# Optimization experiments

Hardware: AMD Instinct MI355X
Metric: run time of the kernel (lower is better)

## Reference

```python
import jax, jax.numpy as jnp
import numpy as np

DT = 1e-3
TAU_MEM_INV = 100.0
TAU_SYN_INV = 200.0
TAU_PRE_INV = 20.0
TAU_POST_INV = 20.0
ETA_PLUS, ETA_MINUS = 0.004, 0.003
W_MIN, W_MAX = 0.0, 1.0


def _dog_kernels():
    # DoGFilter.DoG_kernel(sigma1=1, sigma2=2, size=5): ax = arange(-2, 3)
    ax = jnp.arange(-2.0, 3.0)
    xx, yy = jnp.meshgrid(ax, ax, indexing='ij')
    r2 = xx * xx + yy * yy
    g1 = jnp.exp(-r2 / 2.0)
    g1 = g1 / g1.sum()
    g2 = jnp.exp(-r2 / 8.0)
    g2 = g2 / g2.sum()
    return g1[None, None], g2[None, None]


def _conv(x, w):
    # torch Conv2d (cross-correlation), stride 1, no padding
    return jax.lax.conv_general_dilated(x, w, (1, 1), 'VALID', dimension_numbers=('NCHW', 'OIHW', 'NCHW'))


def _maxpool2(x):
    return jax.lax.reduce_window(x, -jnp.inf, jax.lax.max, (1, 1, 2, 2), (1, 1, 2, 2), 'VALID')


def _unfold(x, k):
    # torch.nn.functional.unfold: [B,C,H,W] -> [B, C*k*k, L], channel-major (c, kh, kw)
    B, C, H, W = x.shape
    Ho, Wo = H - k + 1, W - k + 1
    cols = jnp.stack([x[:, :, i:i + Ho, j:j + Wo] for i in range(k) for j in range(k)], axis=2)
    return cols.reshape(B, C * k * k, Ho * Wo)


def _lif_step(inp, v, i, v_th):
    # norse lif_feed_forward_step (v_leak = v_reset = 0); forward spike = heaviside
    v_dec = v + DT * TAU_MEM_INV * (-v + i)
    i_dec = i - DT * TAU_SYN_INV * i
    z = (v_dec - v_th > 0).astype(inp.dtype)
    return z, (1.0 - z) * v_dec, i_dec + inp


def _stdp_step(z_pre, z_post, w, t_pre, t_post):
    # norse stdp_step_conv2d with stdp_algorithm='multiplicative_relu', mu=0, hard bounds [0,1]
    t_pre = t_pre + DT * TAU_PRE_INV * (-t_pre + z_pre)
    t_post = t_post + DT * TAU_POST_INV * (-t_post + z_post)
    k = w.shape[2]
    B, Co = z_post.shape[0], z_post.shape[1]
    zp = z_post.reshape(B, Co, -1)
    tp = t_post.reshape(B, Co, -1)
    dw_plus = ETA_PLUS * jax.nn.relu(W_MAX - w) * jnp.einsum('bil,bjl->ji', _unfold(t_pre, k), zp).reshape(w.shape)
    dw_minus = ETA_MINUS * jax.nn.relu(w - W_MIN) * jnp.einsum('bil,bjl->ji', _unfold(z_pre, k), tp).reshape(w.shape)
    w = jnp.clip(w + dw_plus - dw_minus, W_MIN, W_MAX)
    return w, t_pre, t_post


def _forward(x, dog_b1, dog_b2, w1, w2, fc1_w, fc1_b, out_w):
    T, B, _, H, _ = x.shape
    g1, g2 = _dog_kernels()
    Hd = H - 4          # DoG output (60)
    H1 = Hd - 4         # conv1 output (56)
    Hp = H1 // 2        # pooled (28)
    H2 = Hp - 4         # conv2 output (24)
    Bf = (B * 100) // 3200  # rows after z4.view(-1, 3200)
    f32 = x.dtype
    z0 = lambda *s: jnp.zeros(s, f32)
    carry = (w1, w2,
             z0(B, 30, H1, H1), z0(B, 30, H1, H1),     # lif0 v, i
             z0(B, 100, H2, H2), z0(B, 100, H2, H2),   # lif1 v, i
             z0(Bf, 500), z0(Bf, 500),                 # lif2 v, i
             z0(Bf, 10), z0(Bf, 10),                   # LI output cell v, i
             z0(B, 2, Hd, Hd), z0(B, 30, H1, H1),      # stdp1 t_pre, t_post
             z0(B, 30, Hp, Hp), z0(B, 100, H2, H2))    # stdp2 t_pre, t_post

    def step(c, xt):
        (w1, w2, v0, i0, v1, i1, v2, i2, vo, io, tp1, tq1, tp2, tq2) = c
        # DoG filter: the two Conv2d biases survive the weight overwrite
        x1 = _conv(xt, g1) + dog_b1
        x2 = _conv(xt, g2) + dog_b2
        z = jnp.concatenate([x1 - x2, x2 - x1], axis=1)   # on/off channels [B,2,Hd,Hd]
        z2 = _conv(z, w1)
        z2, v0, i0 = _lif_step(z2, v0, i0, 15.0)
        w1, tp1, tq1 = _stdp_step(z, z2, w1, tp1, tq1)
        z3 = _maxpool2(z2)
        z4 = 10.0 * _conv(z3, w2)
        z4, v1, i1 = _lif_step(z4, v1, i1, 10.0)
        w2, tp2, tq2 = _stdp_step(z3, z4, w2, tp2, tq2)
        g = jnp.max(z4, axis=(2, 3)).reshape(-1, 3200)    # AdaptiveMaxPool2d(1) + view(-1, 3200)
        h = g @ fc1_w.T + fc1_b
        h, v2, i2 = _lif_step(h, v2, i2, 1.0)
        # LILinearCell (norse li_step), no bias
        i_jump = io + jax.nn.relu(h) @ out_w.T
        vo = vo + DT * TAU_MEM_INV * (-vo + i_jump)
        io = i_jump - DT * TAU_SYN_INV * i_jump
        volt = jnp.broadcast_to(vo, (B, 10))              # voltages[ts] = v (broadcast [1,10] -> [B,10])
        return (w1, w2, v0, i0, v1, i1, v2, i2, vo, io, tp1, tq1, tp2, tq2), volt

    _, voltages = jax.lax.scan(jax.checkpoint(step), carry, x)
    return voltages  # [T, B, 10]


def setup_inputs() -> dict:
    key = jax.random.key(0)
    ks = jax.random.split(key, 7)
    T, B, H = 32, 32, 64
    return {
        'x': jax.random.uniform(ks[0], (T, B, 1, H, H), jnp.float32),
        'dog_b1': jax.random.uniform(ks[1], (1,), jnp.float32, -0.2, 0.2),
        'dog_b2': jax.random.uniform(ks[2], (1,), jnp.float32, -0.2, 0.2),
        'w1': jax.random.normal(ks[3], (30, 2, 5, 5), jnp.float32),
        'w2': jax.random.normal(ks[4], (100, 30, 5, 5), jnp.float32),
        'fc1_w': jax.random.normal(ks[5], (500, 3200), jnp.float32) * 0.02,
        'fc1_b': jnp.zeros((500,), jnp.float32),
        'out_w': jax.random.normal(ks[6], (10, 500), jnp.float32) * float(np.sqrt(2.0 / 500.0)),
    }


def reference(x, dog_b1, dog_b2, w1, w2, fc1_w, fc1_b, out_w):
    return _forward(x, dog_b1, dog_b2, w1, w2, fc1_w, fc1_b, out_w)
```

## Files before the change

### kernel.cpp

```cpp
#include <hip/hip_runtime.h>
#include <math.h>

#define DTMEM 0.1f
#define DTSYN 0.2f
#define DTTR  0.02f

static constexpr int B = 32, T = 32;
static constexpr int HD = 60, HP = 28;
static constexpr int LD = HD*HD, LP = HP*HP;

static constexpr size_t SVI = (size_t)B*8*2*7*448*4;
static constexpr size_t SST = (size_t)B*8*2*7*448*2;
static constexpr size_t S2  = (size_t)B*7*6*384*4;

static constexpr size_t OW1A  = 0;
static constexpr size_t OW1B  = OW1A + 1500;
static constexpr size_t OVI0  = OW1B + 1500;
static constexpr size_t OTQ1  = OVI0 + SVI;
static constexpr size_t OTP2  = OTQ1 + SST;
static constexpr size_t OZ3A  = OTP2 + (size_t)B*30*LP;
static constexpr size_t OZ3B  = OZ3A + (size_t)B*30*LP;
static constexpr size_t OV1S  = OZ3B + (size_t)B*30*LP;
static constexpr size_t OI1S  = OV1S + S2;
static constexpr size_t OTQ2S = OI1S + S2;
static constexpr size_t OPHIA = OTQ2S + S2;
static constexpr size_t OPLOA = OPHIA + 376320;
static constexpr size_t OPZ3A = OPLOA + 376320;
static constexpr size_t OPHIB = OPZ3A + 376320;
static constexpr size_t OPLOB = OPHIB + 376320;
static constexpr size_t OPZ3B = OPLOB + 376320;
static constexpr size_t OZEROEND = OPZ3B + 376320;
static constexpr size_t OZALL  = OZEROEND;
static constexpr size_t OTPALL = OZALL + (size_t)T*B*3600;
static constexpr size_t OEPA  = OTPALL + (size_t)T*B*3600;
static constexpr size_t OEMA  = OEPA + (size_t)B*75000;
static constexpr size_t OEPB  = OEMA + (size_t)B*75000;
static constexpr size_t OEMB  = OEPB + (size_t)B*75000;
static constexpr size_t OPARTA = OEMB + (size_t)B*75000;
static constexpr size_t OPARTB = OPARTA + 96000;
static constexpr size_t OG    = OPARTB + 96000;
static constexpr size_t OHH   = OG + (size_t)T*3200;
static constexpr size_t OW2A  = OHH + (size_t)T*500;
static constexpr size_t OW2B  = OW2A + 84000;
static constexpr size_t OCNZA = OW2B + 84000;
static constexpr size_t OCNZB = OCNZA + 3840;
static constexpr size_t OQZF  = OCNZB + 3840;
static constexpr size_t OPZF  = OQZF + 512;
static constexpr size_t OSZF  = OPZF + 960;
static constexpr size_t OEAA  = OSZF + 224;
static constexpr size_t OEAB  = OEAA + 224;
static constexpr size_t OATH  = OEAB + 224;
static constexpr size_t OATL  = OATH + 516096;
static constexpr size_t OSPK  = OATL + 516096;
static constexpr size_t OEND  = OSPK + 16;

struct DK { float v[25]; };

typedef __attribute__((ext_vector_type(8))) short bfx8;
typedef __attribute__((ext_vector_type(4))) float f32x4;

static __device__ __forceinline__ unsigned short f2bf(float f) {
    unsigned u = __float_as_uint(f);
    return (unsigned short)((u + 0x7FFFu + ((u >> 16) & 1u)) >> 16);
}
static __device__ __forceinline__ float bf2f(unsigned short h) {
    return __uint_as_float(((unsigned)h) << 16);
}

static __device__ __forceinline__ float2 w1pair(const float* w1cur, const float* pprev,
                                                int o, int pp, int t) {
    float wa = w1cur[o*50 + pp], wb = w1cur[o*50 + 25 + pp];
    if (t > 0) {
        float EpS = 0.f, EmS = 0.f;
        for (int s = 0; s < 64; ++s) {
            EpS += pprev[s*1500 + o*50 + pp];
            EmS += pprev[s*1500 + o*50 + 25 + pp];
        }
        wa = fminf(fmaxf(wa + 0.004f*fmaxf(1.f-wa,0.f)*EpS - 0.003f*fmaxf(wa,0.f)*EmS, 0.f), 1.f);
        wb = fminf(fmaxf(wb + 0.004f*fmaxf(1.f-wb,0.f)*(-EpS) - 0.003f*fmaxf(wb,0.f)*(-EmS), 0.f), 1.f);
    }
    return make_float2(wa, wb);
}

static __device__ __forceinline__ float w2eff(float w, int e, int jgg,
        const int* eaR, const float* EPr, const float* EMr) {
    float ep = 0.f, em = 0.f; int any = 0;
    for (int bb = 0; bb < 32; ++bb) {
        if (eaR[bb*7 + jgg]) {
            any = 1;
            ep += EPr[(size_t)bb*75000 + e];
            em += EMr[(size_t)bb*75000 + e];
        }
    }
    if (!any) return w;
    float dwp = 0.004f * fmaxf(1.0f - w, 0.0f) * ep;
    float dwm = 0.003f * fmaxf(w, 0.0f) * em;
    return fminf(fmaxf(w + dwp - dwm, 0.0f), 1.0f);
}

union SMEM {
    struct {
        float zsh[32*60];
        float tsh[32*60];
        float red[700];
        float wd[100];
        float vish[448*4];
        float tqsh[448*2];
        int   sflags[8];
    } f;
    struct {
        union { float spre[LP]; unsigned short sB[10656]; } u;
        unsigned short aTH[8*576], aTL[8*576];
        unsigned int aZ4b[16*18];
        int sjany[16];
        int sany, sAnyTq, ganyJ;
        int sCA[30];
    } v;
};

__global__ __launch_bounds__(384) void k_pre(
        const float* __restrict__ x, const float* __restrict__ b1,
        const float* __restrict__ b2, float* __restrict__ zall,
        float* __restrict__ tpall, DK dk) {
    __shared__ __attribute__((aligned(16))) float xsh[10*64];
    int g = blockIdx.x, b = blockIdx.y, tid = threadIdx.x;
    int r0 = g*6;
    bool valid = tid < 360;
    int lr = tid / 60, col = tid - lr*60;
    float tp = 0.f;
    float bias = b1[0] - b2[0];
    #pragma unroll 1
    for (int t = 0; t < T; ++t) {
        __syncthreads();
        const float4* xs = (const float4*)(x + ((size_t)t*B + b)*4096 + (size_t)r0*64);
        for (int i = tid; i < 160; i += 384) ((float4*)xsh)[i] = xs[i];
        __syncthreads();
        if (valid) {
            float a = 0.f;
            #pragma unroll
            for (int kh = 0; kh < 5; kh++)
                #pragma unroll
                for (int kw = 0; kw < 5; kw++)
                    a = fmaf(dk.v[kh*5+kw], xsh[(lr+kh)*64 + col + kw], a);
            float zv = a + bias;
            tp = tp + DTTR*(zv - tp);
            size_t o = ((size_t)t*B + b)*3600 + (size_t)g*360 + tid;
            zall[o] = zv;
            tpall[o] = tp;
        }
    }
}

__global__ __launch_bounds__(448) void k_sim(
        const float* __restrict__ zall, const float* __restrict__ w1,
        int* __restrict__ spk) {
    __shared__ __attribute__((aligned(16))) float zsh[32*60];
    __shared__ float wd0[100], wdC[100];
    const int og = blockIdx.x & 7, by = blockIdx.x >> 3;
    const int b = by >> 1, yh = by & 1, y0 = yh*28;
    const int tid = threadIdx.x;
    if (tid < 100) {
        int oo2 = tid / 25, pp = tid % 25;
        int o2 = og*4 + oo2; if (o2 > 29) o2 = 29;
        float wa = w1[o2*50 + pp], wb = w1[o2*50 + 25 + pp];
        wd0[tid] = wa - wb;
        wa = fminf(fmaxf(wa, 0.f), 1.f);
        wb = fminf(fmaxf(wb, 0.f), 1.f);
        wdC[tid] = wa - wb;
    }
    int oo = tid & 3, xq = (tid >> 2) & 3, yv = tid >> 4;
    int o = og*4 + oo, xx0 = xq*14;
    bool valid = (o < 30);
    float v[14], ci[14];
    #pragma unroll
    for (int k = 0; k < 14; ++k) { v[k] = 0.f; ci[k] = 0.f; }
    bool any = false;
    #pragma unroll 1
    for (int t = 0; t < T; ++t) {
        __syncthreads();
        const float4* zs = (const float4*)(zall + ((size_t)t*B + b)*3600 + (size_t)y0*60);
        for (int i2 = tid; i2 < 480; i2 += 448) ((float4*)zsh)[i2] = zs[i2];
        __syncthreads();
        if (valid) {
            float acc[14];
            #pragma unroll
            for (int k = 0; k < 14; k++) acc[k] = 0.f;
            const float* wdp = (t == 0) ? wd0 : wdC;
            #pragma unroll
            for (int kh = 0; kh < 5; kh++) {
                float rr[18];
                const float2* r2 = (const float2*)&zsh[(yv+kh)*HD + xx0];
                #pragma unroll
                for (int i = 0; i < 9; i++) ((float2*)rr)[i] = r2[i];
                #pragma unroll
                for (int kw = 0; kw < 5; kw++) {
                    float w = wdp[oo*25 + kh*5 + kw];
                    #pragma unroll
                    for (int k = 0; k < 14; k++) acc[k] = fmaf(w, rr[k+kw], acc[k]);
                }
            }
            #pragma unroll
            for (int e = 0; e < 14; ++e) {
                float vd = v[e] + DTMEM*(ci[e] - v[e]);
                float z = (vd > 15.0f) ? 1.0f : 0.0f;
                any = any || (z != 0.f);
                v[e] = (1.0f - z)*vd;
                ci[e] = (ci[e] - DTSYN*ci[e]) + acc[e];
            }
        }
    }
    if (any) atomicOr(spk, 1);
}

__global__ __launch_bounds__(448) void k_step(float* __restrict__ ws, int t) {
    __shared__ __attribute__((aligned(16))) SMEM sm;
    const int blk = blockIdx.x, tid = threadIdx.x;
    if (((const int*)(ws + OSPK))[0] == 0) return;

    if (blk < 224) {
        const int u = t - 1;
        if (u < 0) return;
        const int cb = blk;
        const int jgg = cb % 7, b = cb / 7, jb0 = jgg*16;
        const float* w2cur = ws + ((u&1) ? OW2B : OW2A);
        float*       w2nxt = ws + ((u&1) ? OW2A : OW2B);
        const float* EPr = ws + ((u&1) ? OEPA : OEPB);
        const float* EMr = ws + ((u&1) ? OEMA : OEMB);
        float*       EPw = ws + ((u&1) ? OEPB : OEPA);
        float*       EMw = ws + ((u&1) ? OEMB : OEMA);
        const int*   eaR = (const int*)(ws + ((u&1) ? OEAA : OEAB));
        int*         eaW = (int*)(ws + ((u&1) ? OEAB : OEAA));
        const int*   cnzP = (const int*)(ws + ((u&1) ? OCNZB : OCNZA));
        const float* z3r = ws + ((u&1) ? OZ3B : OZ3A);
        const unsigned short* uhiR = (const unsigned short*)(ws + ((u&1) ? OPHIB : OPHIA));
        const unsigned short* uloR = (const unsigned short*)(ws + ((u&1) ? OPLOB : OPLOA));
        const unsigned short* uz3R = (const unsigned short*)(ws + ((u&1) ? OPZ3B : OPZ3A));
        unsigned short* gTH = (unsigned short*)(ws + OATH) + (size_t)cb*8*576;
        unsigned short* gTL = (unsigned short*)(ws + OATL) + (size_t)cb*8*576;
        int* szf = (int*)(ws + OSZF);
        float* g_t = ws + OG + (size_t)u*3200;

        if (u < 31) {
            int e = cb*448 + tid;
            if (e < 75000) {
                int j = e/750, r = e - j*750, c = r/25, p25 = r - c*25;
                size_t f = ((size_t)j*30 + c)*28 + p25;
                float w = w2cur[f];
                if (u >= 1) w = w2eff(w, e, j>>4, eaR, EPr, EMr);
                w2nxt[f] = w;
            }
        }

        if (tid == 0) { sm.v.sany = 0; sm.v.sAnyTq = 0; sm.v.ganyJ = 0; }
        if (tid < 16) sm.v.sjany[tid] = 0;
        for (int i2 = tid; i2 < 288; i2 += 448) sm.v.aZ4b[i2] = 0u;
        __syncthreads();
        if (tid < 120 && cnzP[b*120 + tid]) atomicOr(&sm.v.sany, 1);
        if (tid < 30) {
            const int* cz = cnzP + (b*30 + tid)*4;
            sm.v.sCA[tid] = (cz[0] | cz[1] | cz[2] | cz[3]);
        }
        if (u >= 1 && tid < 32 && eaR[tid*7 + jgg]) atomicOr(&sm.v.ganyJ, 1);
        __syncthreads();
        const int szv = szf[b*7 + jgg];
        if (szv && !sm.v.sany) {
            if (tid < 16 && jb0 + tid < 100) g_t[b*100 + jb0 + tid] = 0.f;
            if (u < 31 && tid == 0) eaW[b*7 + jgg] = 0;
            return;
        }
        const bool run = tid < 384;
        int jp = tid & 7, xh = (tid >> 3) & 1, yv = tid >> 4;
        int j0 = jb0 + jp*2;
        int ja = (j0 < 100) ? j0 : 99, jbb = (j0+1 < 100) ? j0+1 : 99;
        int xx0 = xh*12;
        float acc0[12], acc1[12];
        #pragma unroll
        for (int xq = 0; xq < 12; xq++) { acc0[xq] = 0.f; acc1[xq] = 0.f; }
        const int gJ = sm.v.ganyJ;
        #pragma unroll 1
        for (int c = 0; c < 30; ++c) {
            bool act = sm.v.sCA[c] != 0;
            __syncthreads();
            if (act) {
                const float4* src = (const float4*)(z3r + (size_t)(b*30 + c)*LP);
                for (int i2 = tid; i2 < 196; i2 += 448) ((float4*)sm.v.u.spre)[i2] = src[i2];
            }
            __syncthreads();
            if (!act) continue;
            if (run) {
                #pragma unroll 1
                for (int jj = 0; jj < 2; ++jj) {
                    int jc = jj ? jbb : ja;
                    float wa[28];
                    #pragma unroll
                    for (int i = 0; i < 7; i++)
                        ((float4*)wa)[i] = ((const float4*)(w2cur + ((size_t)jc*30 + c)*28))[i];
                    if (u >= 1 && gJ) {
                        #pragma unroll
                        for (int p25 = 0; p25 < 25; p25++)
                            wa[p25] = w2eff(wa[p25], (jc*30 + c)*25 + p25, jc>>4, eaR, EPr, EMr);
                    }
                    float* accp = jj ? acc1 : acc0;
                    #pragma unroll
                    for (int kh = 0; kh < 5; kh++) {
                        float rr[16];
                        const float4* r4 = (const float4*)&sm.v.u.spre[(yv+kh)*HP + xx0];
                        #pragma unroll
                        for (int i = 0; i < 4; i++) ((float4*)rr)[i] = r4[i];
                        #pragma unroll
                        for (int kw = 0; kw < 5; kw++) {
                            float w0 = wa[kh*5+kw];
                            #pragma unroll
                            for (int xq = 0; xq < 12; xq++)
                                accp[xq] = fmaf(w0, rr[xq+kw], accp[xq]);
                        }
                    }
                }
            }
        }
        bool spk0 = false, spk1 = false, anyTq = false;
        if (run) {
            float4* v1p = (float4*)(ws + OV1S);
            float4* i1p = (float4*)(ws + OI1S);
            float4* t2p = (float4*)(ws + OTQ2S);
            size_t sb2 = ((size_t)(b*7 + jgg)*6)*384 + tid;
            #pragma unroll
            for (int jj = 0; jj < 2; jj++) {
                bool anyspk = false;
                int rj = jp*2 + jj;
                #pragma unroll
                for (int i = 0; i < 3; i++) {
                    size_t si = sb2 + (size_t)(jj*3 + i)*384;
                    float4 v4 = v1p[si];
                    float4 c4 = i1p[si];
                    float4 t4 = t2p[si];
                    float4 vn, in, tn4;
                    float* vp=(float*)&v4; float* cp=(float*)&c4; float* tp=(float*)&t4;
                    float* vnp=(float*)&vn; float* inp=(float*)&in; float* tnp=(float*)&tn4;
                    unsigned zb4 = 0;
                    #pragma unroll
                    for (int k = 0; k < 4; k++) {
                        float a = jj ? acc1[i*4+k] : acc0[i*4+k];
                        float vd = vp[k] + DTMEM*(cp[k] - vp[k]);
                        float z = (vd > 10.0f) ? 1.0f : 0.0f;
                        vnp[k] = (1.0f - z)*vd;
                        inp[k] = (cp[k] - DTSYN*cp[k]) + 10.0f*a;
                        tnp[k] = tp[k] + DTTR*(z - tp[k]);
                        if (z != 0.f) { zb4 |= 1u << k; anyspk = true; }
                        anyTq = anyTq || (tnp[k] != 0.f);
                    }
                    v1p[si] = vn;
                    i1p[si] = in;
                    t2p[si] = tn4;
                    int col = yv*24 + xx0 + i*4;
                    if (zb4) atomicOr(&sm.v.aZ4b[rj*18 + (col >> 5)], zb4 << (col & 31));
                    ushort4 hb, lb4;
                    unsigned short h;
                    h = f2bf(tnp[0]); hb.x = h; lb4.x = f2bf(tnp[0] - bf2f(h));
                    h = f2bf(tnp[1]); hb.y = h; lb4.y = f2bf(tnp[1] - bf2f(h));
                    h = f2bf(tnp[2]); hb.z = h; lb4.z = f2bf(tnp[2] - bf2f(h));
                    h = f2bf(tnp[3]); hb.w = h; lb4.w = f2bf(tnp[3] - bf2f(h));
                    if (rj < 8) {
                        *(ushort4*)&sm.v.aTH[rj*576 + col] = hb;
                        *(ushort4*)&sm.v.aTL[rj*576 + col] = lb4;
                    } else {
                        size_t gb = (size_t)(rj - 8)*576 + col;
                        *(ushort4*)(gTH + gb) = hb;
                        *(ushort4*)(gTL + gb) = lb4;
                    }
                }
                if (jj == 0) spk0 = anyspk; else spk1 = anyspk;
            }
            if (spk0 && j0 < 100) atomicOr(&sm.v.sjany[jp*2], 1);
            if (spk1 && j0+1 < 100) atomicOr(&sm.v.sjany[jp*2+1], 1);
            if (anyTq) atomicOr(&sm.v.sAnyTq, 1);
        }
        __syncthreads();
        if (tid < 16 && jb0 + tid < 100) g_t[b*100 + jb0 + tid] = sm.v.sjany[tid] ? 1.f : 0.f;
        if (tid == 0 && szv) szf[b*7 + jgg] = 0;
        if (u < 31) {
            int m0i = 0;
            #pragma unroll
            for (int k = 0; k < 16; k++) m0i |= sm.v.sjany[k];
            bool m0 = (m0i != 0);
            bool mq = (sm.v.sAnyTq != 0);
            bool ea = m0 || mq;
            if (tid == 0) eaW[b*7 + jgg] = ea ? 1 : 0;
            if (!ea) return;
            for (int i2 = tid; i2 < 576; i2 += 448) sm.v.u.sB[10080 + i2] = 0;
            int lane = tid & 63, wv = tid >> 6;
            int mode = wv >> 1, n = wv & 1;
            bool wact = (wv < 4);
            int r = lane & 15;
            bool r8 = (r < 8);
            int g8 = (lane >> 4) * 8;
            int p25 = n*16 + r;
            int offB1, offB2;
            {
                int offH, offL, offZ;
                if (p25 < 25) {
                    int dy = p25/5, dx = p25 - dy*5;
                    offH = ((0*5 + dx)*672 + dy*24)*2;
                    offL = ((1*5 + dx)*672 + dy*24)*2;
                    offZ = ((2*5 + dx)*672 + dy*24)*2;
                } else { offH = offL = offZ = 10080*2; }
                offB1 = (mode == 0) ? offH : offZ;
                offB2 = (mode == 0) ? offL : offZ;
            }
            float* Ew = (mode == 0) ? EPw : EMw;
            const char* sBb = (const char*)sm.v.u.sB;
            #pragma unroll 1
            for (int h = 0; h < 2; ++h) {
                if (h == 1) {
                    __syncthreads();
                    for (int i2 = tid; i2 < 1152; i2 += 448) {
                        if (i2 < 576) ((uint4*)sm.v.aTH)[i2] = ((const uint4*)gTH)[i2];
                        else ((uint4*)sm.v.aTL)[i2-576] = ((const uint4*)gTL)[i2-576];
                    }
                }
                int m0h = sm.v.sjany[h*8+0] | sm.v.sjany[h*8+1] | sm.v.sjany[h*8+2] |
                          sm.v.sjany[h*8+3] | sm.v.sjany[h*8+4] | sm.v.sjany[h*8+5] |
                          sm.v.sjany[h*8+6] | sm.v.sjany[h*8+7];
                #pragma unroll 1
                for (int c = 0; c < 30; ++c) {
                    bool cAc = sm.v.sCA[c] != 0;
                    __syncthreads();
                    {
                        const size_t pbase = (size_t)(b*30 + c)*784;
                        for (int idx = tid; idx < 784; idx += 448) {
                            int rw = idx/28, col = idx - rw*28;
                            #pragma unroll
                            for (int pl = 0; pl < 3; ++pl) {
                                bool need = (pl < 2) ? m0 : (cAc && mq);
                                if (!need) continue;
                                unsigned short vvv =
                                    ((pl == 0) ? uhiR : (pl == 1) ? uloR : uz3R)[pbase + idx];
                                int base = pl*5*672 + rw*24;
                                #pragma unroll
                                for (int dx = 0; dx < 5; ++dx) {
                                    int xx = col - dx;
                                    if (xx >= 0 && xx < 24) sm.v.u.sB[base + dx*672 + xx] = vvv;
                                }
                            }
                        }
                    }
                    __syncthreads();
                    if (!wact) continue;
                    f32x4 C = (f32x4){0.f, 0.f, 0.f, 0.f};
                    bool go = (mode == 0) ? (m0h != 0) : (mq && cAc);
                    if (go) {
                        for (int ks = 0; ks < 18; ++ks) {
                            int kk = ks*32 + g8;
                            bfx8 a1 = {}, a2 = {};
                            if (mode == 0) {
                                unsigned wbits = 0;
                                if (r8) wbits = sm.v.aZ4b[(h*8 + r)*18 + ks] >> g8;
                                #pragma unroll
                                for (int k = 0; k < 8; ++k)
                                    ((short*)&a1)[k] = ((wbits >> k) & 1u) ? (short)0x3F80 : (short)0;
                                a2 = a1;
                            } else if (r8) {
                                a1 = *(const bfx8*)(sm.v.aTH + r*576 + ks*32);
                                a2 = *(const bfx8*)(sm.v.aTL + r*576 + ks*32);
                            }
                            bfx8 b1v = *(const bfx8*)(sBb + offB1 + kk*2);
                            bfx8 b2v = *(const bfx8*)(sBb + offB2 + kk*2);
                            C = __builtin_amdgcn_mfma_f32_16x16x32_bf16(a1, b1v, C, 0, 0, 0);
                            C = __builtin_amdgcn_mfma_f32_16x16x32_bf16(a2, b2v, C, 0, 0, 0);
                        }
                    }
                    if (p25 < 25 && (lane >> 4) < 2) {
                        #pragma unroll
                        for (int q = 0; q < 4; ++q) {
                            int j = jb0 + h*8 + (lane >> 4)*4 + q;
                            if (j < 100)
                                Ew[(size_t)b*75000 + ((size_t)j*30 + c)*25 + p25] = C[q];
                        }
                    }
                }
            }
        }
        return;
    }

    if (t >= T) return;
    const int fb = blk - 224;
    const int og = fb & 7, by = fb >> 3;
    const int b = by >> 1, yh = by & 1, y0 = yh*28;

    const float* w1cur = ws + ((t&1) ? OW1B : OW1A);
    float*       w1nxt = ws + ((t&1) ? OW1A : OW1B);
    float*       partW = ws + ((t&1) ? OPARTB : OPARTA);
    const float* pprev = ws + ((t&1) ? OPARTA : OPARTB);
    int*         cnzW  = (int*)(ws + ((t&1) ? OCNZB : OCNZA));
    float*       z3W   = ws + ((t&1) ? OZ3B : OZ3A);
    unsigned short* uhiW = (unsigned short*)(ws + ((t&1) ? OPHIB : OPHIA));
    unsigned short* uloW = (unsigned short*)(ws + ((t&1) ? OPLOB : OPLOA));
    unsigned short* uz3W = (unsigned short*)(ws + ((t&1) ? OPZ3B : OPZ3A));
    float* vi0g = ws + OVI0; float* tq1g = ws + OTQ1;
    float* tp2g = ws + OTP2;
    int* qzf = (int*)(ws + OQZF);
    int* pzf = (int*)(ws + OPZF);

    const int prow = (b*2 + yh)*1500;
    int qzOld = qzf[(b*8 + og)*2 + yh];
    size_t sb = ((size_t)((b*8 + og)*2 + yh)*7)*448 + tid;
    float4* vi0p = (float4*)vi0g;
    float2* tq1p = (float2*)tq1g;
    {
        const float4* zs = (const float4*)(ws + OZALL + ((size_t)t*B + b)*3600 + (size_t)y0*60);
        const float4* ts = (const float4*)(ws + OTPALL + ((size_t)t*B + b)*3600 + (size_t)y0*60);
        for (int i2 = tid; i2 < 480; i2 += 448) {
            ((float4*)sm.f.zsh)[i2] = zs[i2];
            ((float4*)sm.f.tsh)[i2] = ts[i2];
        }
        #pragma unroll
        for (int i = 0; i < 7; i++)
            ((float4*)sm.f.vish)[i*448 + tid] = vi0p[sb + (size_t)i*448];
        if (!qzOld) {
            #pragma unroll
            for (int i = 0; i < 7; i++)
                ((float2*)sm.f.tqsh)[i*448 + tid] = tq1p[sb + (size_t)i*448];
        }
    }
    if (tid < 100) {
        int oo2 = tid / 25, pp = tid % 25;
        int o2 = og*4 + oo2; if (o2 > 29) o2 = 29;
        float2 wp = w1pair(w1cur, pprev, o2, pp, t);
        sm.f.wd[tid] = wp.x - wp.y;
    }
    if (fb < 4) {
        int e = fb*448 + tid;
        if (e < 1500) {
            int o = e/50, r = e%50, ch = r/25, pp = r%25;
            float2 wp = w1pair(w1cur, pprev, o, pp, t);
            w1nxt[e] = ch ? wp.y : wp.x;
        }
    }
    if (tid < 8) sm.f.sflags[tid] = 0;
    __syncthreads();
    int oo = tid & 3, xq = (tid >> 2) & 3, yv = tid >> 4;
    int o = og*4 + oo, xx0 = xq*14;
    bool valid = (o < 30);
    unsigned zmask = 0;
    float qs = 0.f;
    bool anym = false;
    if (valid) {
        float acc[14];
        #pragma unroll
        for (int k = 0; k < 14; k++) acc[k] = 0.f;
        #pragma unroll
        for (int kh = 0; kh < 5; kh++) {
            float rr[18];
            const float2* r2 = (const float2*)&sm.f.zsh[(yv+kh)*HD + xx0];
            #pragma unroll
            for (int i = 0; i < 9; i++) ((float2*)rr)[i] = r2[i];
            #pragma unroll
            for (int kw = 0; kw < 5; kw++) {
                float w = sm.f.wd[oo*25 + kh*5 + kw];
                #pragma unroll
                for (int k = 0; k < 14; k++) acc[k] = fmaf(w, rr[k+kw], acc[k]);
            }
        }
        #pragma unroll
        for (int i = 0; i < 7; i++) {
            float4 vi = ((float4*)sm.f.vish)[i*448 + tid];
            float2 t2;
            if (qzOld) { t2.x = 0.f; t2.y = 0.f; }
            else t2 = ((float2*)sm.f.tqsh)[i*448 + tid];
            float4 vin;
            float2 tn2;
            bool sp = false;
            #pragma unroll
            for (int k = 0; k < 2; k++) {
                int e = i*2 + k;
                float vv = k ? vi.y : vi.x, cc = k ? vi.w : vi.z, tt = k ? t2.y : t2.x;
                float vd = vv + DTMEM*(cc - vv);
                float z = (vd > 15.0f) ? 1.0f : 0.0f;
                float vo = (1.0f - z)*vd;
                float io_ = (cc - DTSYN*cc) + acc[e];
                float tq = tt + DTTR*(z - tt);
                if (k) { vin.y = vo; vin.w = io_; tn2.y = tq; }
                else   { vin.x = vo; vin.z = io_; tn2.x = tq; }
                if (z != 0.f) { zmask |= 1u << e; sp = true; }
                qs += tq;
            }
            vi0p[sb + (size_t)i*448] = vin;
            ((float2*)sm.f.tqsh)[i*448 + tid] = tn2;
            if (!qzOld || sp) tq1p[sb + (size_t)i*448] = tn2;
        }
        float mx[7];
        #pragma unroll
        for (int k = 0; k < 7; k++) mx[k] = ((zmask >> (2*k)) & 3u) ? 1.0f : 0.0f;
        #pragma unroll
        for (int k = 0; k < 7; k++) {
            float pm = __shfl_xor(mx[k], 16, 64);
            mx[k] = fmaxf(mx[k], pm);
        }
        if ((yv & 1) == 0) {
            int pzOld = pzf[b*30 + o];
            int py = yh*14 + (yv >> 1);
            size_t pb = ((size_t)(b*30 + o)*HP + py)*HP + xq*7;
            #pragma unroll
            for (int k = 0; k < 7; k++) {
                float m = mx[k];
                anym = anym || (m != 0.f);
                if (!pzOld || m != 0.f) {
                    z3W[pb + k] = m;
                    float tpv = pzOld ? 0.f : tp2g[pb + k];
                    float tnew = tpv + DTTR*(m - tpv);
                    tp2g[pb + k] = tnew;
                    unsigned short h = f2bf(tnew);
                    uhiW[pb + k] = h;
                    uloW[pb + k] = f2bf(tnew - bf2f(h));
                    uz3W[pb + k] = (m != 0.f) ? (unsigned short)0x3F80 : (unsigned short)0;
                }
            }
        }
    }
    if (anym) atomicOr(&sm.f.sflags[oo*2 + (xq >> 1)], 1);
    __syncthreads();
    int anyblk = sm.f.sflags[0]|sm.f.sflags[1]|sm.f.sflags[2]|sm.f.sflags[3]|
                 sm.f.sflags[4]|sm.f.sflags[5]|sm.f.sflags[6]|sm.f.sflags[7];
    if (tid < 8) {
        int o2 = og*4 + (tid >> 1);
        if (o2 < 30) cnzW[(b*30 + o2)*4 + yh*2 + (tid & 1)] = sm.f.sflags[tid];
    }
    if (tid < 4) {
        int o2 = og*4 + tid;
        if (o2 < 30 && (sm.f.sflags[tid*2] | sm.f.sflags[tid*2+1])) pzf[b*30 + o2] = 0;
    }
    if (tid == 0 && qzOld && anyblk) qzf[(b*8 + og)*2 + yh] = 0;

    if (qzOld && !anyblk) {
        if (tid < 100) {
            int oo2 = tid / 25, q = tid % 25;
            int o2 = og*4 + oo2;
            if (o2 < 30) {
                partW[prow + o2*50 + q] = 0.f;
                partW[prow + o2*50 + 25 + q] = 0.f;
            }
        }
        return;
    }
    int lane = tid & 63, wave = tid >> 6;
    {
        float a[25];
        #pragma unroll
        for (int pq = 0; pq < 25; pq++) a[pq] = 0.f;
        if (valid && qs != 0.f) {
            float tn[14];
            #pragma unroll
            for (int i = 0; i < 7; i++) {
                float2 t2 = ((float2*)sm.f.tqsh)[i*448 + tid];
                tn[2*i] = t2.x; tn[2*i+1] = t2.y;
            }
            #pragma unroll
            for (int kh = 0; kh < 5; kh++) {
                float rr[18];
                const float2* r2 = (const float2*)&sm.f.zsh[(yv+kh)*HD + xx0];
                #pragma unroll
                for (int i = 0; i < 9; i++) ((float2*)rr)[i] = r2[i];
                #pragma unroll
                for (int kw = 0; kw < 5; kw++)
                    #pragma unroll
                    for (int k = 0; k < 14; k++)
                        a[kh*5+kw] = fmaf(rr[k+kw], tn[k], a[kh*5+kw]);
            }
        }
        #pragma unroll
        for (int q = 0; q < 25; q++) {
            float v = a[q];
            v += __shfl_xor(v, 4, 64);
            v += __shfl_xor(v, 8, 64);
            v += __shfl_xor(v, 16, 64);
            v += __shfl_xor(v, 32, 64);
            if (lane < 4) sm.f.red[wave*100 + lane*25 + q] = v;
        }
    }
    __syncthreads();
    if (tid < 100) {
        int oo2 = tid / 25, q = tid % 25;
        float s = 0.f;
        #pragma unroll
        for (int w = 0; w < 7; w++) s += sm.f.red[w*100 + oo2*25 + q];
        int o2 = og*4 + oo2;
        if (o2 < 30) partW[prow + o2*50 + 25 + q] = s;
    }
    __syncthreads();
    {
        float a[25];
        #pragma unroll
        for (int pq = 0; pq < 25; pq++) a[pq] = 0.f;
        if (valid && zmask != 0u) {
            float zf[14];
            #pragma unroll
            for (int k = 0; k < 14; k++) zf[k] = ((zmask >> k) & 1u) ? 1.0f : 0.0f;
            #pragma unroll
            for (int kh = 0; kh < 5; kh++) {
                float rr[18];
                const float2* r2 = (const float2*)&sm.f.tsh[(yv+kh)*HD + xx0];
                #pragma unroll
                for (int i = 0; i < 9; i++) ((float2*)rr)[i] = r2[i];
                #pragma unroll
                for (int kw = 0; kw < 5; kw++)
                    #pragma unroll
                    for (int k = 0; k < 14; k++)
                        a[kh*5+kw] = fmaf(rr[k+kw], zf[k], a[kh*5+kw]);
            }
        }
        #pragma unroll
        for (int q = 0; q < 25; q++) {
            float v = a[q];
            v += __shfl_xor(v, 4, 64);
            v += __shfl_xor(v, 8, 64);
            v += __shfl_xor(v, 16, 64);
            v += __shfl_xor(v, 32, 64);
            if (lane < 4) sm.f.red[wave*100 + lane*25 + q] = v;
        }
    }
    __syncthreads();
    if (tid < 100) {
        int oo2 = tid / 25, q = tid % 25;
        float s = 0.f;
        #pragma unroll
        for (int w = 0; w < 7; w++) s += sm.f.red[w*100 + oo2*25 + q];
        int o2 = og*4 + oo2;
        if (o2 < 30) partW[prow + o2*50 + q] = s;
    }
}

__global__ void k_prep(const float* __restrict__ w2, float* __restrict__ w2p,
                       int* __restrict__ qzf, int* __restrict__ pzf,
                       int* __restrict__ szf, int* __restrict__ spk) {
    int e = blockIdx.x*blockDim.x + threadIdx.x;
    if (e < 75000) {
        int j = e / 750, r = e % 750, c = r / 25, p = r % 25;
        w2p[((size_t)j*30 + c)*28 + p] = w2[e];
    }
    if (e < 512) qzf[e] = 1;
    if (e < 960) pzf[e] = 1;
    if (e < 224) szf[e] = 1;
    if (e < 4) spk[e] = 0;
}

__global__ __launch_bounds__(256) void k_fc1b(
        const float* __restrict__ g_all, const float* __restrict__ fcw,
        const float* __restrict__ fcb, float* __restrict__ h_all) {
    __shared__ float red[8][4];
    int n = blockIdx.x, by = blockIdx.y, tid = threadIdx.x;
    const float4* w4 = (const float4*)(fcw + (size_t)n*3200);
    float4 wreg[4];
    #pragma unroll
    for (int i = 0; i < 4; i++) {
        int k = tid + 256*i;
        if (k < 800) wreg[i] = w4[k];
    }
    float accs[8];
    #pragma unroll
    for (int tt = 0; tt < 8; tt++) accs[tt] = 0.f;
    #pragma unroll 1
    for (int tt = 0; tt < 8; tt++) {
        int t = by*8 + tt;
        const float4* g4 = (const float4*)(g_all + (size_t)t*3200);
        float a = 0.f;
        #pragma unroll
        for (int i = 0; i < 4; i++) {
            int k = tid + 256*i;
            if (k < 800) {
                float4 gv = g4[k];
                a = fmaf(gv.x, wreg[i].x, a);
                a = fmaf(gv.y, wreg[i].y, a);
                a = fmaf(gv.z, wreg[i].z, a);
                a = fmaf(gv.w, wreg[i].w, a);
            }
        }
        accs[tt] = a;
    }
    int lane = tid & 63, wid = tid >> 6;
    #pragma unroll
    for (int tt = 0; tt < 8; tt++) {
        float v = accs[tt];
        #pragma unroll
        for (int s = 32; s >= 1; s >>= 1) v += __shfl_down(v, s, 64);
        if (lane == 0) red[tt][wid] = v;
    }
    __syncthreads();
    if (tid < 8)
        h_all[(size_t)(by*8 + tid)*500 + n] =
            red[tid][0] + red[tid][1] + red[tid][2] + red[tid][3] + fcb[n];
}

__global__ __launch_bounds__(640) void k_head_all(
        const float* __restrict__ h_all, const float* __restrict__ outw,
        float* __restrict__ out) {
    __shared__ float spk[500];
    __shared__ float vout[10];
    int tid = threadIdx.x;
    int wid = tid >> 6, lane = tid & 63;
    float v2r = 0.f, i2r = 0.f;
    float vor = 0.f, ior = 0.f;
    #pragma unroll 1
    for (int t = 0; t < 32; t++) {
        if (tid < 500) {
            float cur = i2r;
            float vd = v2r + DTMEM*(cur - v2r);
            float z = (vd > 1.0f) ? 1.0f : 0.0f;
            v2r = (1.0f - z)*vd;
            i2r = (cur - DTSYN*cur) + h_all[t*500 + tid];
            spk[tid] = z;
        }
        __syncthreads();
        float acc = 0.f;
        for (int n = lane; n < 500; n += 64)
            acc = fmaf(spk[n], outw[wid*500 + n], acc);
        #pragma unroll
        for (int s = 32; s >= 1; s >>= 1) acc += __shfl_down(acc, s, 64);
        if (lane == 0) {
            float ij = ior + acc;
            float vn = vor + DTMEM*(ij - vor);
            ior = ij - DTSYN*ij;
            vor = vn;
            vout[wid] = vn;
        }
        __syncthreads();
        if (tid < 320) out[(size_t)t*320 + tid] = vout[tid % 10];
        __syncthreads();
    }
}

extern "C" void kernel_launch(void* const* d_in, const int* in_sizes, int n_in,
                              void* d_out, int out_size, void* d_ws, size_t ws_size,
                              hipStream_t stream) {
    const float* x    = (const float*)d_in[0];
    const float* b1   = (const float*)d_in[1];
    const float* b2   = (const float*)d_in[2];
    const float* w1   = (const float*)d_in[3];
    const float* w2   = (const float*)d_in[4];
    const float* fcw  = (const float*)d_in[5];
    const float* fcb  = (const float*)d_in[6];
    const float* outw = (const float*)d_in[7];
    float* ws  = (float*)d_ws;
    float* out = (float*)d_out;

    DK dk;
    {
        float g1[25], g2[25], s1 = 0.f, s2 = 0.f;
        for (int i = 0; i < 5; i++)
            for (int j = 0; j < 5; j++) {
                float ai = (float)(i - 2), aj = (float)(j - 2);
                float r2 = ai*ai + aj*aj;
                g1[i*5+j] = expf(-r2/2.0f);
                g2[i*5+j] = expf(-r2/8.0f);
                s1 += g1[i*5+j]; s2 += g2[i*5+j];
            }
        for (int k = 0; k < 25; k++) dk.v[k] = g1[k]/s1 - g2[k]/s2;
    }

    hipMemcpyAsync(ws + OW1A, w1, 1500*sizeof(float), hipMemcpyDeviceToDevice, stream);
    hipMemsetAsync(ws + OVI0, 0, (OZEROEND - OVI0)*sizeof(float), stream);
    hipMemsetAsync(ws + OG, 0, (size_t)T*3200*sizeof(float), stream);
    k_prep<<<294, 256, 0, stream>>>(w2, ws + OW2A, (int*)(ws + OQZF),
                                    (int*)(ws + OPZF), (int*)(ws + OSZF),
                                    (int*)(ws + OSPK));
    k_pre<<<dim3(10, 32), 384, 0, stream>>>(x, b1, b2, ws + OZALL, ws + OTPALL, dk);
    k_sim<<<512, 448, 0, stream>>>(ws + OZALL, ws + OW1A, (int*)(ws + OSPK));

    for (int t = 0; t <= T; ++t)
        k_step<<<736, 448, 0, stream>>>(ws, t);

    k_fc1b<<<dim3(500, 4), 256, 0, stream>>>(ws + OG, fcw, fcb, ws + OHH);
    k_head_all<<<1, 640, 0, stream>>>(ws + OHH, outw, out);
}
```

Before: 338.9 us.

## Gate state zeroing, prep and fc1 on spike flag; double-buffer pre/sim kernels

The spike simulation now runs before state initialisation. The large workspace memset becomes a k_zero kernel that exits when layer 1 produced no spikes. k_prep and k_fc1b also exit early in that case, and k_fc1b then writes just the bias, which matches the result when there is no downstream activity. k_pre and k_sim double-buffer their per-timestep shared-memory tiles, which removes one barrier per step, and k_sim uses 896 threads with 7 outputs each instead of 14. The skip relies on a device-side flag, so the work saved depends on the input, and the reordering adds one extra kernel launch.

```diff
diff --git a/kernel.cpp b/kernel.cpp
--- a/kernel.cpp
+++ b/kernel.cpp
@@ -122,39 +122,46 @@
         const float* __restrict__ x, const float* __restrict__ b1,
         const float* __restrict__ b2, float* __restrict__ zall,
         float* __restrict__ tpall, DK dk) {
-    __shared__ __attribute__((aligned(16))) float xsh[10*64];
+    __shared__ __attribute__((aligned(16))) float xsh[2][10*64];
     int g = blockIdx.x, b = blockIdx.y, tid = threadIdx.x;
     int r0 = g*6;
     bool valid = tid < 360;
     int lr = tid / 60, col = tid - lr*60;
     float tp = 0.f;
     float bias = b1[0] - b2[0];
+    if (tid < 160) {
+        const float4* xs = (const float4*)(x + ((size_t)b)*4096 + (size_t)r0*64);
+        ((float4*)xsh[0])[tid] = xs[tid];
+    }
+    __syncthreads();
     #pragma unroll 1
     for (int t = 0; t < T; ++t) {
-        __syncthreads();
-        const float4* xs = (const float4*)(x + ((size_t)t*B + b)*4096 + (size_t)r0*64);
-        for (int i = tid; i < 160; i += 384) ((float4*)xsh)[i] = xs[i];
-        __syncthreads();
+        const float* xc = xsh[t & 1];
+        if (t + 1 < T && tid < 160) {
+            const float4* xs = (const float4*)(x + ((size_t)(t+1)*B + b)*4096 + (size_t)r0*64);
+            ((float4*)xsh[(t+1) & 1])[tid] = xs[tid];
+        }
         if (valid) {
             float a = 0.f;
             #pragma unroll
             for (int kh = 0; kh < 5; kh++)
                 #pragma unroll
                 for (int kw = 0; kw < 5; kw++)
-                    a = fmaf(dk.v[kh*5+kw], xsh[(lr+kh)*64 + col + kw], a);
+                    a = fmaf(dk.v[kh*5+kw], xc[(lr+kh)*64 + col + kw], a);
             float zv = a + bias;
             tp = tp + DTTR*(zv - tp);
             size_t o = ((size_t)t*B + b)*3600 + (size_t)g*360 + tid;
             zall[o] = zv;
             tpall[o] = tp;
         }
-    }
-}
-
-__global__ __launch_bounds__(448) void k_sim(
+        __syncthreads();
+    }
+}
+
+__global__ __launch_bounds__(896) void k_sim(
         const float* __restrict__ zall, const float* __restrict__ w1,
         int* __restrict__ spk) {
-    __shared__ __attribute__((aligned(16))) float zsh[32*60];
+    __shared__ __attribute__((aligned(16))) float zsh[2][1920];
     __shared__ float wd0[100], wdC[100];
     const int og = blockIdx.x & 7, by = blockIdx.x >> 3;
     const int b = by >> 1, yh = by & 1, y0 = yh*28;
@@ -164,43 +171,50 @@
         int o2 = og*4 + oo2; if (o2 > 29) o2 = 29;
         float wa = w1[o2*50 + pp], wb = w1[o2*50 + 25 + pp];
         wd0[tid] = wa - wb;
-        wa = fminf(fmaxf(wa, 0.f), 1.f);
-        wb = fminf(fmaxf(wb, 0.f), 1.f);
-        wdC[tid] = wa - wb;
-    }
-    int oo = tid & 3, xq = (tid >> 2) & 3, yv = tid >> 4;
-    int o = og*4 + oo, xx0 = xq*14;
+        wdC[tid] = fminf(fmaxf(wa, 0.f), 1.f) - fminf(fmaxf(wb, 0.f), 1.f);
+    }
+    int oo = tid & 3, xq = (tid >> 2) & 7, yv = tid >> 5;
+    int o = og*4 + oo;
     bool valid = (o < 30);
-    float v[14], ci[14];
+    int c0 = xq*7;
+    int cb2 = c0 & ~1;
+    int off = c0 & 1;
+    float v[7], ci[7];
     #pragma unroll
-    for (int k = 0; k < 14; ++k) { v[k] = 0.f; ci[k] = 0.f; }
+    for (int k = 0; k < 7; ++k) { v[k] = 0.f; ci[k] = 0.f; }
     bool any = false;
+    if (tid < 480) {
+        const float4* zs = (const float4*)(zall + ((size_t)b)*3600 + (size_t)y0*60);
+        ((float4*)zsh[0])[tid] = zs[tid];
+    }
+    __syncthreads();
     #pragma unroll 1
     for (int t = 0; t < T; ++t) {
-        __syncthreads();
-        const float4* zs = (const float4*)(zall + ((size_t)t*B + b)*3600 + (size_t)y0*60);
-        for (int i2 = tid; i2 < 480; i2 += 448) ((float4*)zsh)[i2] = zs[i2];
-        __syncthreads();
+        const float* zc = zsh[t & 1];
+        if (t + 1 < T && tid < 480) {
+            const float4* zs = (const float4*)(zall + ((size_t)(t+1)*B + b)*3600 + (size_t)y0*60);
+            ((float4*)zsh[(t+1) & 1])[tid] = zs[tid];
+        }
         if (valid) {
-            float acc[14];
-            #pragma unroll
-            for (int k = 0; k < 14; k++) acc[k] = 0.f;
+            float acc[7];
+            #pragma unroll
+            for (int k = 0; k < 7; k++) acc[k] = 0.f;
             const float* wdp = (t == 0) ? wd0 : wdC;
             #pragma unroll
             for (int kh = 0; kh < 5; kh++) {
-                float rr[18];
-                const float2* r2 = (const float2*)&zsh[(yv+kh)*HD + xx0];
+                float rr[12];
+                const float2* r2 = (const float2*)&zc[(yv+kh)*HD + cb2];
                 #pragma unroll
-                for (int i = 0; i < 9; i++) ((float2*)rr)[i] = r2[i];
+                for (int i = 0; i < 6; i++) ((float2*)rr)[i] = r2[i];
                 #pragma unroll
                 for (int kw = 0; kw < 5; kw++) {
                     float w = wdp[oo*25 + kh*5 + kw];
                     #pragma unroll
-                    for (int k = 0; k < 14; k++) acc[k] = fmaf(w, rr[k+kw], acc[k]);
+                    for (int k = 0; k < 7; k++) acc[k] = fmaf(w, rr[off + k + kw], acc[k]);
                 }
             }
             #pragma unroll
-            for (int e = 0; e < 14; ++e) {
+            for (int e = 0; e < 7; ++e) {
                 float vd = v[e] + DTMEM*(ci[e] - v[e]);
                 float z = (vd > 15.0f) ? 1.0f : 0.0f;
                 any = any || (z != 0.f);
@@ -208,8 +222,19 @@
                 ci[e] = (ci[e] - DTSYN*ci[e]) + acc[e];
             }
         }
+        __syncthreads();
     }
     if (any) atomicOr(spk, 1);
+}
+
+__global__ __launch_bounds__(256) void k_zero(float* __restrict__ ws) {
+    if (((const int*)(ws + OSPK))[0] == 0) return;
+    const size_t n = (OZEROEND - OVI0) / 4;
+    float4* p = (float4*)(ws + OVI0);
+    float4 z; z.x = 0.f; z.y = 0.f; z.z = 0.f; z.w = 0.f;
+    for (size_t i = (size_t)blockIdx.x*blockDim.x + threadIdx.x; i < n;
+         i += (size_t)gridDim.x*blockDim.x)
+        p[i] = z;
 }
 
 __global__ __launch_bounds__(448) void k_step(float* __restrict__ ws, int t) {
@@ -732,7 +757,8 @@
 
 __global__ void k_prep(const float* __restrict__ w2, float* __restrict__ w2p,
                        int* __restrict__ qzf, int* __restrict__ pzf,
-                       int* __restrict__ szf, int* __restrict__ spk) {
+                       int* __restrict__ szf, const int* __restrict__ spk) {
+    if (spk[0] == 0) return;
     int e = blockIdx.x*blockDim.x + threadIdx.x;
     if (e < 75000) {
         int j = e / 750, r = e % 750, c = r / 25, p = r % 25;
@@ -741,14 +767,18 @@
     if (e < 512) qzf[e] = 1;
     if (e < 960) pzf[e] = 1;
     if (e < 224) szf[e] = 1;
-    if (e < 4) spk[e] = 0;
 }
 
 __global__ __launch_bounds__(256) void k_fc1b(
         const float* __restrict__ g_all, const float* __restrict__ fcw,
-        const float* __restrict__ fcb, float* __restrict__ h_all) {
+        const float* __restrict__ fcb, float* __restrict__ h_all,
+        const int* __restrict__ spk) {
     __shared__ float red[8][4];
     int n = blockIdx.x, by = blockIdx.y, tid = threadIdx.x;
+    if (spk[0] == 0) {
+        if (tid < 8) h_all[(size_t)(by*8 + tid)*500 + n] = fcb[n];
+        return;
+    }
     const float4* w4 = (const float4*)(fcw + (size_t)n*3200);
     float4 wreg[4];
     #pragma unroll
@@ -858,17 +888,19 @@
     }
 
     hipMemcpyAsync(ws + OW1A, w1, 1500*sizeof(float), hipMemcpyDeviceToDevice, stream);
-    hipMemsetAsync(ws + OVI0, 0, (OZEROEND - OVI0)*sizeof(float), stream);
+    hipMemsetAsync(ws + OSPK, 0, 16*sizeof(float), stream);
     hipMemsetAsync(ws + OG, 0, (size_t)T*3200*sizeof(float), stream);
+    k_pre<<<dim3(10, 32), 384, 0, stream>>>(x, b1, b2, ws + OZALL, ws + OTPALL, dk);
+    k_sim<<<512, 896, 0, stream>>>(ws + OZALL, ws + OW1A, (int*)(ws + OSPK));
+    k_zero<<<1024, 256, 0, stream>>>(ws);
     k_prep<<<294, 256, 0, stream>>>(w2, ws + OW2A, (int*)(ws + OQZF),
                                     (int*)(ws + OPZF), (int*)(ws + OSZF),
-                                    (int*)(ws + OSPK));
-    k_pre<<<dim3(10, 32), 384, 0, stream>>>(x, b1, b2, ws + OZALL, ws + OTPALL, dk);
-    k_sim<<<512, 448, 0, stream>>>(ws + OZALL, ws + OW1A, (int*)(ws + OSPK));
+                                    (const int*)(ws + OSPK));
 
     for (int t = 0; t <= T; ++t)
         k_step<<<736, 448, 0, stream>>>(ws, t);
 
-    k_fc1b<<<dim3(500, 4), 256, 0, stream>>>(ws + OG, fcw, fcb, ws + OHH);
+    k_fc1b<<<dim3(500, 4), 256, 0, stream>>>(ws + OG, fcw, fcb, ws + OHH,
+                                             (const int*)(ws + OSPK));
     k_head_all<<<1, 640, 0, stream>>>(ws + OHH, outw, out);
 }
```

Result: slower. 586.4 us (+73.0%).
